# Kernel optimization log

Measured on AMD Instinct MI355X. Metric: run time of the kernel, lower is better.

The kernel has to match this reference:

```python
import jax, jax.numpy as jnp
import numpy as np

EMBED = 512  # scale uses embed_size**-0.5 per the original forward (NOT head_size)


def setup_inputs() -> dict:
    key = jax.random.key(0)
    k1, k2, k3, k4 = jax.random.split(key, 4)
    B, T, D, H = 8, 4096, EMBED, 64
    inputs = jax.random.normal(k1, (B, T, D), dtype=jnp.float32)
    Wq = jax.random.normal(k2, (D, H), dtype=jnp.float32) * (D ** -0.5)
    Wk = jax.random.normal(k3, (D, H), dtype=jnp.float32) * (D ** -0.5)
    Wv = jax.random.normal(k4, (D, H), dtype=jnp.float32) * (D ** -0.5)
    return {"inputs": inputs, "Wq": Wq, "Wk": Wk, "Wv": Wv}


def reference(inputs, Wq, Wk, Wv):
    # inputs: [B, T, D]; Wq/Wk/Wv: [D, H]
    B, T, D = inputs.shape
    q = inputs @ Wq  # [B, T, H]
    k = inputs @ Wk  # [B, T, H]
    v = inputs @ Wv  # [B, T, H]
    scale = jnp.asarray(D, inputs.dtype) ** -0.5  # original scales by embed_size**-0.5
    scores = jnp.einsum('bth,bsh->bts', q, k) * scale  # [B, T, T]
    causal = jnp.arange(T)[:, None] >= jnp.arange(T)[None, :]  # lower-triangular
    scores = jnp.where(causal, scores, jnp.asarray(-jnp.inf, scores.dtype))
    weights = jax.nn.softmax(scores, axis=-1)
    # dropout is identity in eval mode
    return weights @ v  # [B, T, H]
```

## Files before the change

kernel.cpp:

```cpp
#include <hip/hip_runtime.h>
#include <hip/hip_bf16.h>
#include <math.h>

#define TSEQ 4096
#define NB 8
#define DEM 512
#define HD 64
#define KP 66
#define VP 34
#define WIP 136
#define WIMG 26624
#define QSZ ((size_t)NB * TSEQ * HD)
#define SLOTS_PER_B 144

typedef __attribute__((ext_vector_type(8))) short short8;
typedef __attribute__((ext_vector_type(4))) short short4v;
typedef __attribute__((ext_vector_type(4))) float float4v;
typedef __attribute__((ext_vector_type(16))) float f32x16;

__device__ __forceinline__ short f2bf(float f) {
    union { float f; unsigned u; } v; v.f = f;
    unsigned r = v.u + 0x7fffu + ((v.u >> 16) & 1u);
    return (short)(r >> 16);
}

__device__ __forceinline__ short8 pack8(float4 a, float4 b) {
    union { short8 s; __hip_bfloat162 h[4]; } u;
    u.h[0] = __float22bfloat162_rn(make_float2(a.x, a.y));
    u.h[1] = __float22bfloat162_rn(make_float2(a.z, a.w));
    u.h[2] = __float22bfloat162_rn(make_float2(b.x, b.y));
    u.h[3] = __float22bfloat162_rn(make_float2(b.z, b.w));
    return u.s;
}

__device__ __forceinline__ int pkbf2(float x, float y) {
    union { __hip_bfloat162 h; int i; } u;
    u.h = __float22bfloat162_rn(make_float2(x, y));
    return u.i;
}

__device__ __forceinline__ short8 mk8(int a, int b, int c, int d) {
    union { short8 s; int i[4]; } u;
    u.i[0] = a; u.i[1] = b; u.i[2] = c; u.i[3] = d;
    return u.s;
}

__device__ __forceinline__ void gload_lds16(const void* g, void* l) {
    __builtin_amdgcn_global_load_lds(
        (const __attribute__((address_space(1))) unsigned int*)g,
        (__attribute__((address_space(3))) unsigned int*)l,
        16, 0, 0);
}

__device__ __host__ __forceinline__ int slot_base(int mq) {
    int a = mq >> 2, r = mq & 3;
    return (a + 1) * (2 * a + r);
}

__global__ __launch_bounds__(256) void wtr_kernel(
    const float* __restrict__ Wq, const float* __restrict__ Wk,
    const float* __restrict__ Wv, short* __restrict__ wimg)
{
    __shared__ float t[64][65];
    const int tid = threadIdx.x;
    const int kb = blockIdx.x;
    const int k0 = kb * 64;
    const int m = blockIdx.y;
    const int c = kb >> 1, half = kb & 1;
    const float* W = (m == 0) ? Wq : ((m == 1) ? Wk : Wv);
    const float sc = (m == 0) ? (0.044194173824159216f * 1.4426950408889634f)
                              : 1.0f;

#pragma unroll
    for (int i = 0; i < 4; ++i) {
        int f = tid + 256 * i;
        int k = f >> 4, n4 = (f & 15) * 4;
        float4 wv = *(const float4*)&W[(k0 + k) * HD + n4];
        t[k][n4 + 0] = wv.x; t[k][n4 + 1] = wv.y;
        t[k][n4 + 2] = wv.z; t[k][n4 + 3] = wv.w;
    }
    __syncthreads();
#pragma unroll
    for (int i = 0; i < 4; ++i) {
        int f = tid + 256 * i;
        int n = f >> 4, k4 = (f & 15) * 4;
        short4v o;
        o[0] = f2bf(t[k4 + 0][n] * sc);
        o[1] = f2bf(t[k4 + 1][n] * sc);
        o[2] = f2bf(t[k4 + 2][n] * sc);
        o[3] = f2bf(t[k4 + 3][n] * sc);
        *(short4v*)&wimg[c * WIMG + (64 * m + n) * WIP + half * 64 + k4] = o;
    }
}

__global__ __launch_bounds__(256, 3) void qkv_mfma(
    const float* __restrict__ x, const short* __restrict__ wimg,
    short* __restrict__ q, short* __restrict__ k, short* __restrict__ vt)
{
    __shared__ alignas(16) short wlds[WIMG];

    const int tid = threadIdx.x;
    const int w = tid >> 6;
    const int l15 = tid & 15;
    const int quad = (tid >> 4) & 3;
    const int rbase = blockIdx.x * 64 + w * 16 + l15;

    const float* xr = x + (size_t)rbase * DEM;
    float4v acc[12] = {};

    float4 xa[4], xb[4];
#pragma unroll
    for (int ks = 0; ks < 4; ++ks) {
        xa[ks] = *(const float4*)&xr[ks * 32 + quad * 8];
        xb[ks] = *(const float4*)&xr[ks * 32 + quad * 8 + 4];
    }

    for (int c = 0; c < 4; ++c) {
        __syncthreads();
        {
            const char* gsrc = (const char*)(wimg + c * WIMG) + tid * 16;
            char* ldst = (char*)wlds + tid * 16;
#pragma unroll
            for (int i = 0; i < 13; ++i)
                gload_lds16(gsrc + i * 4096, ldst + i * 4096);
        }
        short8 xv[4];
#pragma unroll
        for (int ks = 0; ks < 4; ++ks) xv[ks] = pack8(xa[ks], xb[ks]);
        __syncthreads();

        if (c + 1 < 4) {
#pragma unroll
            for (int ks = 0; ks < 4; ++ks) {
                xa[ks] = *(const float4*)&xr[(c + 1) * 128 + ks * 32 + quad * 8];
                xb[ks] = *(const float4*)&xr[(c + 1) * 128 + ks * 32 + quad * 8 + 4];
            }
        }

#pragma unroll
        for (int ks = 0; ks < 4; ++ks) {
            const int lk = ks * 32 + quad * 8;
#pragma unroll
            for (int mt = 0; mt < 12; ++mt) {
                short8 wf = *(const short8*)&wlds[(mt * 16 + l15) * WIP + lk];
                acc[mt] = __builtin_amdgcn_mfma_f32_16x16x32_bf16(wf, xv[ks], acc[mt], 0, 0, 0);
            }
        }
    }

#pragma unroll
    for (int mt = 0; mt < 8; ++mt) {
        short* dst = (mt < 4) ? q : k;
        short4v o;
        o[0] = f2bf(acc[mt][0]); o[1] = f2bf(acc[mt][1]);
        o[2] = f2bf(acc[mt][2]); o[3] = f2bf(acc[mt][3]);
        *(short4v*)&dst[(size_t)rbase * HD + (mt & 3) * 16 + quad * 4] = o;
    }
    const int b = rbase >> 12, t = rbase & (TSEQ - 1);
#pragma unroll
    for (int mt = 8; mt < 12; ++mt) {
#pragma unroll
        for (int reg = 0; reg < 4; ++reg) {
            int d = (mt - 8) * 16 + quad * 4 + reg;
            vt[((size_t)(b * HD + d)) * TSEQ + t] = f2bf(acc[mt][reg]);
        }
    }
}

__global__ __launch_bounds__(64, 3) void flash_mfma(
    const short* __restrict__ qw, const short* __restrict__ kw,
    const short* __restrict__ vtw, float* __restrict__ out,
    float* __restrict__ pO, float* __restrict__ stS)
{
    __shared__ short kt[32 * KP];
    __shared__ short vl[64 * VP];

    const int lane = threadIdx.x;
    const int q5 = lane & 31;
    const int hi = lane >> 5;
    const int bx = blockIdx.x;
    const int b = bx & 7;
    const int r = bx >> 3;
    const int w = r & 3;
    const int idx = r >> 2;

    int mq, j;
    if (idx < 120) {
        int t = idx;
        mq = 31; j = 0;
#pragma unroll 1
        for (int mm = 31; mm >= 3; --mm) {
            int f = (mm + 1) >> 2;
            if (t < f) { mq = mm; j = t; break; }
            t -= f;
        }
    } else {
        int t = idx - 120;
        int kc = t >> 3, p = t & 7;
        mq = (30 - kc) - 4 * p;
        j = (mq + 1) >> 2;
    }
    const int r0 = mq * 128;
    const int ss0 = 16 * j;
    const int ssend = min(16 * (j + 1), 4 * mq + w + 1);
    const int slot = b * SLOTS_PER_B + slot_base(mq) + j;
    const int qrow = r0 + w * 32 + q5;

    short8 qf[4];
    {
        const short* qp = qw + ((size_t)(b * TSEQ + qrow)) * HD + hi * 8;
#pragma unroll
        for (int ks = 0; ks < 4; ++ks) qf[ks] = *(const short8*)(qp + ks * 16);
    }

    f32x16 O0 = {}, O1 = {};
    float l_lane = 0.f;

    const short* kbase = kw + (size_t)b * TSEQ * HD;
    const short* vbase = vtw + (size_t)b * HD * TSEQ;
    const int krow = lane >> 3, kc8 = (lane & 7) * 8;
    const int vrow = lane >> 2, vc8 = (lane & 3) * 8;

    short8 pk0, pk1, pk2, pk3, pv0, pv1, pv2, pv3;
    {
        const short* kg = kbase + (size_t)(ss0 * 32) * HD;
        const short* vg = vbase + ss0 * 32;
        pk0 = *(const short8*)(kg + (krow +  0) * HD + kc8);
        pk1 = *(const short8*)(kg + (krow +  8) * HD + kc8);
        pk2 = *(const short8*)(kg + (krow + 16) * HD + kc8);
        pk3 = *(const short8*)(kg + (krow + 24) * HD + kc8);
        pv0 = *(const short8*)(vg + (size_t)(vrow +  0) * TSEQ + vc8);
        pv1 = *(const short8*)(vg + (size_t)(vrow + 16) * TSEQ + vc8);
        pv2 = *(const short8*)(vg + (size_t)(vrow + 32) * TSEQ + vc8);
        pv3 = *(const short8*)(vg + (size_t)(vrow + 48) * TSEQ + vc8);
    }

    for (int ss = ss0; ss < ssend; ++ss) {
        __syncthreads();
        *(short8*)&kt[(krow +  0) * KP + kc8] = pk0;
        *(short8*)&kt[(krow +  8) * KP + kc8] = pk1;
        *(short8*)&kt[(krow + 16) * KP + kc8] = pk2;
        *(short8*)&kt[(krow + 24) * KP + kc8] = pk3;
        *(short8*)&vl[(vrow +  0) * VP + vc8] = pv0;
        *(short8*)&vl[(vrow + 16) * VP + vc8] = pv1;
        *(short8*)&vl[(vrow + 32) * VP + vc8] = pv2;
        *(short8*)&vl[(vrow + 48) * VP + vc8] = pv3;
        __syncthreads();

        if (ss + 1 < ssend) {
            const short* kg = kbase + (size_t)((ss + 1) * 32) * HD;
            const short* vg = vbase + (ss + 1) * 32;
            pk0 = *(const short8*)(kg + (krow +  0) * HD + kc8);
            pk1 = *(const short8*)(kg + (krow +  8) * HD + kc8);
            pk2 = *(const short8*)(kg + (krow + 16) * HD + kc8);
            pk3 = *(const short8*)(kg + (krow + 24) * HD + kc8);
            pv0 = *(const short8*)(vg + (size_t)(vrow +  0) * TSEQ + vc8);
            pv1 = *(const short8*)(vg + (size_t)(vrow + 16) * TSEQ + vc8);
            pv2 = *(const short8*)(vg + (size_t)(vrow + 32) * TSEQ + vc8);
            pv3 = *(const short8*)(vg + (size_t)(vrow + 48) * TSEQ + vc8);
        }

        f32x16 S = {};
#pragma unroll
        for (int ks = 0; ks < 4; ++ks) {
            short8 a = *(const short8*)&kt[q5 * KP + ks * 16 + hi * 8];
            S = __builtin_amdgcn_mfma_f32_32x32x16_bf16(a, qf[ks], S, 0, 0, 0);
        }

        if (ss * 32 + 31 > r0 + w * 32) {
#pragma unroll
            for (int reg = 0; reg < 16; ++reg) {
                int key = ss * 32 + (reg & 3) + 8 * (reg >> 2) + 4 * hi;
                if (key > qrow) S[reg] = -INFINITY;
            }
        }

        float p[16];
#pragma unroll
        for (int reg = 0; reg < 16; ++reg) {
            p[reg] = __builtin_amdgcn_exp2f(S[reg]);
            l_lane += p[reg];
        }
        int dd[4][2];
#pragma unroll
        for (int a = 0; a < 4; ++a) {
            dd[a][0] = pkbf2(p[4 * a + 0], p[4 * a + 1]);
            dd[a][1] = pkbf2(p[4 * a + 2], p[4 * a + 3]);
        }
        int ra0 = __shfl_xor(hi ? dd[0][0] : dd[1][0], 32, 64);
        int ra1 = __shfl_xor(hi ? dd[0][1] : dd[1][1], 32, 64);
        int rb0 = __shfl_xor(hi ? dd[2][0] : dd[3][0], 32, 64);
        int rb1 = __shfl_xor(hi ? dd[2][1] : dd[3][1], 32, 64);
        short8 PA0 = hi ? mk8(ra0, ra1, dd[1][0], dd[1][1])
                        : mk8(dd[0][0], dd[0][1], ra0, ra1);
        short8 PA1 = hi ? mk8(rb0, rb1, dd[3][0], dd[3][1])
                        : mk8(dd[2][0], dd[2][1], rb0, rb1);

#pragma unroll
        for (int kr = 0; kr < 2; ++kr) {
            short8 pa = kr ? PA1 : PA0;
            short8 v0 = *(const short8*)&vl[(q5)      * VP + kr * 16 + hi * 8];
            short8 v1 = *(const short8*)&vl[(32 + q5) * VP + kr * 16 + hi * 8];
            O0 = __builtin_amdgcn_mfma_f32_32x32x16_bf16(pa, v0, O0, 0, 0, 0);
            O1 = __builtin_amdgcn_mfma_f32_32x32x16_bf16(pa, v1, O1, 0, 0, 0);
        }
    }

    const float ltot = l_lane + __shfl_xor(l_lane, 32, 64);

    if (mq <= 3) {
        float inv = 1.0f / ltot;
#pragma unroll
        for (int reg = 0; reg < 16; ++reg) {
            int qloc = (reg & 3) + 8 * (reg >> 2) + 4 * hi;
            float ir = __shfl(inv, qloc, 64);
            size_t rowb = (size_t)(b * TSEQ + r0 + w * 32 + qloc) * HD + q5;
            out[rowb]      = O0[reg] * ir;
            out[rowb + 32] = O1[reg] * ir;
        }
    } else {
        float* dest = pO + ((size_t)slot * 128 + w * 32) * HD + q5;
#pragma unroll
        for (int reg = 0; reg < 16; ++reg) {
            int qloc = (reg & 3) + 8 * (reg >> 2) + 4 * hi;
            dest[(size_t)qloc * HD]      = O0[reg];
            dest[(size_t)qloc * HD + 32] = O1[reg];
        }
        if (hi == 0) stS[slot * 128 + w * 32 + q5] = ltot;
    }
}

__global__ __launch_bounds__(256) void merge_kernel(
    float* __restrict__ out, const float* __restrict__ pO,
    const float* __restrict__ stS)
{
    const int tid = threadIdx.x;
    const int bx = blockIdx.x;
    const int b = bx / 56, loc = bx - b * 56;
    const int t = 512 + loc * 64 + (tid >> 2);
    const int dq = (tid & 3) * 16;
    const int mq = t >> 7, rr = t & 127;
    const int nseg = (mq + 4) >> 2;
    const int sb = b * SLOTS_PER_B + slot_base(mq);

    float denom = 0.f;
    for (int s = 0; s < nseg; ++s) denom += stS[(sb + s) * 128 + rr];
    float inv = 1.0f / denom;

    float4 o[4] = {};
    for (int s = 0; s < nseg; ++s) {
        const float4* pp = (const float4*)
            &pO[((size_t)(sb + s) * 128 + rr) * HD + dq];
#pragma unroll
        for (int i = 0; i < 4; ++i) {
            float4 p = pp[i];
            o[i].x += p.x; o[i].y += p.y;
            o[i].z += p.z; o[i].w += p.w;
        }
    }
    float4* op = (float4*)&out[((size_t)b * TSEQ + t) * HD + dq];
#pragma unroll
    for (int i = 0; i < 4; ++i) {
        o[i].x *= inv; o[i].y *= inv; o[i].z *= inv; o[i].w *= inv;
        op[i] = o[i];
    }
}

extern "C" void kernel_launch(void* const* d_in, const int* in_sizes, int n_in,
                              void* d_out, int out_size, void* d_ws, size_t ws_size,
                              hipStream_t stream) {
    const float* x  = (const float*)d_in[0];
    const float* Wq = (const float*)d_in[1];
    const float* Wk = (const float*)d_in[2];
    const float* Wv = (const float*)d_in[3];
    float* out = (float*)d_out;

    short* q  = (short*)d_ws;
    short* k  = q + QSZ;
    short* vt = k + QSZ;
    short* wimg = vt + QSZ;
    float* pO = (float*)(wimg + 4 * WIMG);
    float* stS = pO + (size_t)NB * SLOTS_PER_B * 128 * HD;

    wtr_kernel<<<dim3(8, 3), 256, 0, stream>>>(Wq, Wk, Wv, wimg);
    qkv_mfma<<<dim3(NB * TSEQ / 64), 256, 0, stream>>>(x, wimg, q, k, vt);
    flash_mfma<<<dim3(NB * SLOTS_PER_B * 4), 64, 0, stream>>>(q, k, vt, out, pO, stS);
    merge_kernel<<<dim3(448), 256, 0, stream>>>(out, pO, stS);
}
```

Before: 154.4 us.

## Process two 32-row query groups per flash wavefront to reuse K/V tiles

Each single-wave flash block now handles 64 query rows (two 32-row groups) instead of 32. Each staged K and V tile in LDS is reused for two QK and PV MFMA passes, and the grid is halved. This removes half of the global K/V loads and LDS staging per query, at the cost of doubled accumulator registers (the occupancy hint is dropped), fewer blocks, and some extra masked work on diagonal tiles.

```diff
diff --git a/kernel.cpp b/kernel.cpp
--- a/kernel.cpp
+++ b/kernel.cpp
@@ -167,7 +167,7 @@
     }
 }
 
-__global__ __launch_bounds__(64, 3) void flash_mfma(
+__global__ __launch_bounds__(64) void flash_mfma(
     const short* __restrict__ qw, const short* __restrict__ kw,
     const short* __restrict__ vtw, float* __restrict__ out,
     float* __restrict__ pO, float* __restrict__ stS)
@@ -181,8 +181,8 @@
     const int bx = blockIdx.x;
     const int b = bx & 7;
     const int r = bx >> 3;
-    const int w = r & 3;
-    const int idx = r >> 2;
+    const int w = r & 1;
+    const int idx = r >> 1;
 
     int mq, j;
     if (idx < 120) {
@@ -202,19 +202,19 @@
     }
     const int r0 = mq * 128;
     const int ss0 = 16 * j;
-    const int ssend = min(16 * (j + 1), 4 * mq + w + 1);
+    const int ssend = min(16 * (j + 1), 4 * mq + 2 * w + 2);
     const int slot = b * SLOTS_PER_B + slot_base(mq) + j;
-    const int qrow = r0 + w * 32 + q5;
-
-    short8 qf[4];
-    {
-        const short* qp = qw + ((size_t)(b * TSEQ + qrow)) * HD + hi * 8;
-#pragma unroll
-        for (int ks = 0; ks < 4; ++ks) qf[ks] = *(const short8*)(qp + ks * 16);
-    }
-
-    f32x16 O0 = {}, O1 = {};
-    float l_lane = 0.f;
+
+    short8 qf[2][4];
+#pragma unroll
+    for (int g = 0; g < 2; ++g) {
+        const short* qp = qw + ((size_t)(b * TSEQ + r0 + 64 * w + 32 * g + q5)) * HD + hi * 8;
+#pragma unroll
+        for (int ks = 0; ks < 4; ++ks) qf[g][ks] = *(const short8*)(qp + ks * 16);
+    }
+
+    f32x16 O[2][2] = {};
+    float l_lane[2] = {0.f, 0.f};
 
     const short* kbase = kw + (size_t)b * TSEQ * HD;
     const short* vbase = vtw + (size_t)b * HD * TSEQ;
@@ -260,73 +260,88 @@
             pv3 = *(const short8*)(vg + (size_t)(vrow + 48) * TSEQ + vc8);
         }
 
-        f32x16 S = {};
-#pragma unroll
-        for (int ks = 0; ks < 4; ++ks) {
-            short8 a = *(const short8*)&kt[q5 * KP + ks * 16 + hi * 8];
-            S = __builtin_amdgcn_mfma_f32_32x32x16_bf16(a, qf[ks], S, 0, 0, 0);
-        }
-
-        if (ss * 32 + 31 > r0 + w * 32) {
+#pragma unroll
+        for (int g = 0; g < 2; ++g) {
+            const int grow = r0 + 64 * w + 32 * g;
+            const int qg = grow + q5;
+
+            f32x16 S = {};
+#pragma unroll
+            for (int ks = 0; ks < 4; ++ks) {
+                short8 a = *(const short8*)&kt[q5 * KP + ks * 16 + hi * 8];
+                S = __builtin_amdgcn_mfma_f32_32x32x16_bf16(a, qf[g][ks], S, 0, 0, 0);
+            }
+
+            if (ss * 32 + 31 > grow) {
+#pragma unroll
+                for (int reg = 0; reg < 16; ++reg) {
+                    int key = ss * 32 + (reg & 3) + 8 * (reg >> 2) + 4 * hi;
+                    if (key > qg) S[reg] = -INFINITY;
+                }
+            }
+
+            float p[16];
 #pragma unroll
             for (int reg = 0; reg < 16; ++reg) {
-                int key = ss * 32 + (reg & 3) + 8 * (reg >> 2) + 4 * hi;
-                if (key > qrow) S[reg] = -INFINITY;
-            }
-        }
-
-        float p[16];
-#pragma unroll
-        for (int reg = 0; reg < 16; ++reg) {
-            p[reg] = __builtin_amdgcn_exp2f(S[reg]);
-            l_lane += p[reg];
-        }
-        int dd[4][2];
-#pragma unroll
-        for (int a = 0; a < 4; ++a) {
-            dd[a][0] = pkbf2(p[4 * a + 0], p[4 * a + 1]);
-            dd[a][1] = pkbf2(p[4 * a + 2], p[4 * a + 3]);
-        }
-        int ra0 = __shfl_xor(hi ? dd[0][0] : dd[1][0], 32, 64);
-        int ra1 = __shfl_xor(hi ? dd[0][1] : dd[1][1], 32, 64);
-        int rb0 = __shfl_xor(hi ? dd[2][0] : dd[3][0], 32, 64);
-        int rb1 = __shfl_xor(hi ? dd[2][1] : dd[3][1], 32, 64);
-        short8 PA0 = hi ? mk8(ra0, ra1, dd[1][0], dd[1][1])
-                        : mk8(dd[0][0], dd[0][1], ra0, ra1);
-        short8 PA1 = hi ? mk8(rb0, rb1, dd[3][0], dd[3][1])
-                        : mk8(dd[2][0], dd[2][1], rb0, rb1);
-
-#pragma unroll
-        for (int kr = 0; kr < 2; ++kr) {
-            short8 pa = kr ? PA1 : PA0;
-            short8 v0 = *(const short8*)&vl[(q5)      * VP + kr * 16 + hi * 8];
-            short8 v1 = *(const short8*)&vl[(32 + q5) * VP + kr * 16 + hi * 8];
-            O0 = __builtin_amdgcn_mfma_f32_32x32x16_bf16(pa, v0, O0, 0, 0, 0);
-            O1 = __builtin_amdgcn_mfma_f32_32x32x16_bf16(pa, v1, O1, 0, 0, 0);
-        }
-    }
-
-    const float ltot = l_lane + __shfl_xor(l_lane, 32, 64);
+                p[reg] = __builtin_amdgcn_exp2f(S[reg]);
+                l_lane[g] += p[reg];
+            }
+            int dd[4][2];
+#pragma unroll
+            for (int a = 0; a < 4; ++a) {
+                dd[a][0] = pkbf2(p[4 * a + 0], p[4 * a + 1]);
+                dd[a][1] = pkbf2(p[4 * a + 2], p[4 * a + 3]);
+            }
+            int ra0 = __shfl_xor(hi ? dd[0][0] : dd[1][0], 32, 64);
+            int ra1 = __shfl_xor(hi ? dd[0][1] : dd[1][1], 32, 64);
+            int rb0 = __shfl_xor(hi ? dd[2][0] : dd[3][0], 32, 64);
+            int rb1 = __shfl_xor(hi ? dd[2][1] : dd[3][1], 32, 64);
+            short8 PA0 = hi ? mk8(ra0, ra1, dd[1][0], dd[1][1])
+                            : mk8(dd[0][0], dd[0][1], ra0, ra1);
+            short8 PA1 = hi ? mk8(rb0, rb1, dd[3][0], dd[3][1])
+                            : mk8(dd[2][0], dd[2][1], rb0, rb1);
+
+#pragma unroll
+            for (int kr = 0; kr < 2; ++kr) {
+                short8 pa = kr ? PA1 : PA0;
+                short8 v0 = *(const short8*)&vl[(q5)      * VP + kr * 16 + hi * 8];
+                short8 v1 = *(const short8*)&vl[(32 + q5) * VP + kr * 16 + hi * 8];
+                O[g][0] = __builtin_amdgcn_mfma_f32_32x32x16_bf16(pa, v0, O[g][0], 0, 0, 0);
+                O[g][1] = __builtin_amdgcn_mfma_f32_32x32x16_bf16(pa, v1, O[g][1], 0, 0, 0);
+            }
+        }
+    }
+
+    float ltot[2];
+#pragma unroll
+    for (int g = 0; g < 2; ++g)
+        ltot[g] = l_lane[g] + __shfl_xor(l_lane[g], 32, 64);
 
     if (mq <= 3) {
-        float inv = 1.0f / ltot;
-#pragma unroll
-        for (int reg = 0; reg < 16; ++reg) {
-            int qloc = (reg & 3) + 8 * (reg >> 2) + 4 * hi;
-            float ir = __shfl(inv, qloc, 64);
-            size_t rowb = (size_t)(b * TSEQ + r0 + w * 32 + qloc) * HD + q5;
-            out[rowb]      = O0[reg] * ir;
-            out[rowb + 32] = O1[reg] * ir;
+#pragma unroll
+        for (int g = 0; g < 2; ++g) {
+            float inv = 1.0f / ltot[g];
+#pragma unroll
+            for (int reg = 0; reg < 16; ++reg) {
+                int qloc = (reg & 3) + 8 * (reg >> 2) + 4 * hi;
+                float ir = __shfl(inv, qloc, 64);
+                size_t rowb = (size_t)(b * TSEQ + r0 + 64 * w + 32 * g + qloc) * HD + q5;
+                out[rowb]      = O[g][0][reg] * ir;
+                out[rowb + 32] = O[g][1][reg] * ir;
+            }
         }
     } else {
-        float* dest = pO + ((size_t)slot * 128 + w * 32) * HD + q5;
-#pragma unroll
-        for (int reg = 0; reg < 16; ++reg) {
-            int qloc = (reg & 3) + 8 * (reg >> 2) + 4 * hi;
-            dest[(size_t)qloc * HD]      = O0[reg];
-            dest[(size_t)qloc * HD + 32] = O1[reg];
-        }
-        if (hi == 0) stS[slot * 128 + w * 32 + q5] = ltot;
+#pragma unroll
+        for (int g = 0; g < 2; ++g) {
+            float* dest = pO + ((size_t)slot * 128 + w * 64 + 32 * g) * HD + q5;
+#pragma unroll
+            for (int reg = 0; reg < 16; ++reg) {
+                int qloc = (reg & 3) + 8 * (reg >> 2) + 4 * hi;
+                dest[(size_t)qloc * HD]      = O[g][0][reg];
+                dest[(size_t)qloc * HD + 32] = O[g][1][reg];
+            }
+            if (hi == 0) stS[slot * 128 + w * 64 + 32 * g + q5] = ltot[g];
+        }
     }
 }
 
@@ -384,6 +399,6 @@
 
     wtr_kernel<<<dim3(8, 3), 256, 0, stream>>>(Wq, Wk, Wv, wimg);
     qkv_mfma<<<dim3(NB * TSEQ / 64), 256, 0, stream>>>(x, wimg, q, k, vt);
-    flash_mfma<<<dim3(NB * SLOTS_PER_B * 4), 64, 0, stream>>>(q, k, vt, out, pO, stS);
+    flash_mfma<<<dim3(NB * SLOTS_PER_B * 2), 64, 0, stream>>>(q, k, vt, out, pO, stS);
     merge_kernel<<<dim3(448), 256, 0, stream>>>(out, pO, stS);
 }
```

New measurement: 157.8 us. 1.02x slower.

## Load K/V fragments directly from global into registers, drop LDS staging

Applied to the files above, without the earlier changes.

The flash attention loop no longer stages K and V tiles through shared memory with two barriers per step. Each lane instead loads its MFMA operand fragments straight from global memory into registers, using a two-buffer ping-pong to prefetch the next tile while the current one is computed. The launch-bounds occupancy hint is also relaxed. This removes the LDS traffic and __syncthreads overhead. In exchange it adds more register pressure and gives up the wide coalesced global loads the cooperative staging provided; for V the per-lane 16-byte loads are strided by TSEQ.

```diff
diff --git a/kernel.cpp b/kernel.cpp
--- a/kernel.cpp
+++ b/kernel.cpp
@@ -6,8 +6,6 @@
 #define NB 8
 #define DEM 512
 #define HD 64
-#define KP 66
-#define VP 34
 #define WIP 136
 #define WIMG 26624
 #define QSZ ((size_t)NB * TSEQ * HD)
@@ -167,14 +165,11 @@
     }
 }
 
-__global__ __launch_bounds__(64, 3) void flash_mfma(
+__global__ __launch_bounds__(64) void flash_mfma(
     const short* __restrict__ qw, const short* __restrict__ kw,
     const short* __restrict__ vtw, float* __restrict__ out,
     float* __restrict__ pO, float* __restrict__ stS)
 {
-    __shared__ short kt[32 * KP];
-    __shared__ short vl[64 * VP];
-
     const int lane = threadIdx.x;
     const int q5 = lane & 31;
     const int hi = lane >> 5;
@@ -216,56 +211,31 @@
     f32x16 O0 = {}, O1 = {};
     float l_lane = 0.f;
 
-    const short* kbase = kw + (size_t)b * TSEQ * HD;
-    const short* vbase = vtw + (size_t)b * HD * TSEQ;
-    const int krow = lane >> 3, kc8 = (lane & 7) * 8;
-    const int vrow = lane >> 2, vc8 = (lane & 3) * 8;
-
-    short8 pk0, pk1, pk2, pk3, pv0, pv1, pv2, pv3;
-    {
-        const short* kg = kbase + (size_t)(ss0 * 32) * HD;
-        const short* vg = vbase + ss0 * 32;
-        pk0 = *(const short8*)(kg + (krow +  0) * HD + kc8);
-        pk1 = *(const short8*)(kg + (krow +  8) * HD + kc8);
-        pk2 = *(const short8*)(kg + (krow + 16) * HD + kc8);
-        pk3 = *(const short8*)(kg + (krow + 24) * HD + kc8);
-        pv0 = *(const short8*)(vg + (size_t)(vrow +  0) * TSEQ + vc8);
-        pv1 = *(const short8*)(vg + (size_t)(vrow + 16) * TSEQ + vc8);
-        pv2 = *(const short8*)(vg + (size_t)(vrow + 32) * TSEQ + vc8);
-        pv3 = *(const short8*)(vg + (size_t)(vrow + 48) * TSEQ + vc8);
-    }
-
-    for (int ss = ss0; ss < ssend; ++ss) {
-        __syncthreads();
-        *(short8*)&kt[(krow +  0) * KP + kc8] = pk0;
-        *(short8*)&kt[(krow +  8) * KP + kc8] = pk1;
-        *(short8*)&kt[(krow + 16) * KP + kc8] = pk2;
-        *(short8*)&kt[(krow + 24) * KP + kc8] = pk3;
-        *(short8*)&vl[(vrow +  0) * VP + vc8] = pv0;
-        *(short8*)&vl[(vrow + 16) * VP + vc8] = pv1;
-        *(short8*)&vl[(vrow + 32) * VP + vc8] = pv2;
-        *(short8*)&vl[(vrow + 48) * VP + vc8] = pv3;
-        __syncthreads();
-
-        if (ss + 1 < ssend) {
-            const short* kg = kbase + (size_t)((ss + 1) * 32) * HD;
-            const short* vg = vbase + (ss + 1) * 32;
-            pk0 = *(const short8*)(kg + (krow +  0) * HD + kc8);
-            pk1 = *(const short8*)(kg + (krow +  8) * HD + kc8);
-            pk2 = *(const short8*)(kg + (krow + 16) * HD + kc8);
-            pk3 = *(const short8*)(kg + (krow + 24) * HD + kc8);
-            pv0 = *(const short8*)(vg + (size_t)(vrow +  0) * TSEQ + vc8);
-            pv1 = *(const short8*)(vg + (size_t)(vrow + 16) * TSEQ + vc8);
-            pv2 = *(const short8*)(vg + (size_t)(vrow + 32) * TSEQ + vc8);
-            pv3 = *(const short8*)(vg + (size_t)(vrow + 48) * TSEQ + vc8);
-        }
-
+    const short* kfb  = kw  + ((size_t)(b * TSEQ) + q5) * HD + hi * 8;
+    const short* vfb0 = vtw + ((size_t)(b * HD + q5)) * TSEQ + hi * 8;
+    const short* vfb1 = vtw + ((size_t)(b * HD + 32 + q5)) * TSEQ + hi * 8;
+
+    short8 ka[4], va[4], kb_[4], vb_[4];
+
+    auto LOADF = [&](short8* kf, short8* vf, int ss) {
+        const short* kp  = kfb  + (size_t)ss * 32 * HD;
+        const short* vp0 = vfb0 + ss * 32;
+        const short* vp1 = vfb1 + ss * 32;
+        kf[0] = *(const short8*)(kp);
+        kf[1] = *(const short8*)(kp + 16);
+        kf[2] = *(const short8*)(kp + 32);
+        kf[3] = *(const short8*)(kp + 48);
+        vf[0] = *(const short8*)(vp0);
+        vf[1] = *(const short8*)(vp0 + 16);
+        vf[2] = *(const short8*)(vp1);
+        vf[3] = *(const short8*)(vp1 + 16);
+    };
+
+    auto STEP = [&](const short8* kf, const short8* vf, int ss) {
         f32x16 S = {};
 #pragma unroll
-        for (int ks = 0; ks < 4; ++ks) {
-            short8 a = *(const short8*)&kt[q5 * KP + ks * 16 + hi * 8];
-            S = __builtin_amdgcn_mfma_f32_32x32x16_bf16(a, qf[ks], S, 0, 0, 0);
-        }
+        for (int ks = 0; ks < 4; ++ks)
+            S = __builtin_amdgcn_mfma_f32_32x32x16_bf16(kf[ks], qf[ks], S, 0, 0, 0);
 
         if (ss * 32 + 31 > r0 + w * 32) {
 #pragma unroll
@@ -296,15 +266,22 @@
         short8 PA1 = hi ? mk8(rb0, rb1, dd[3][0], dd[3][1])
                         : mk8(dd[2][0], dd[2][1], rb0, rb1);
 
-#pragma unroll
-        for (int kr = 0; kr < 2; ++kr) {
-            short8 pa = kr ? PA1 : PA0;
-            short8 v0 = *(const short8*)&vl[(q5)      * VP + kr * 16 + hi * 8];
-            short8 v1 = *(const short8*)&vl[(32 + q5) * VP + kr * 16 + hi * 8];
-            O0 = __builtin_amdgcn_mfma_f32_32x32x16_bf16(pa, v0, O0, 0, 0, 0);
-            O1 = __builtin_amdgcn_mfma_f32_32x32x16_bf16(pa, v1, O1, 0, 0, 0);
-        }
-    }
+        O0 = __builtin_amdgcn_mfma_f32_32x32x16_bf16(PA0, vf[0], O0, 0, 0, 0);
+        O0 = __builtin_amdgcn_mfma_f32_32x32x16_bf16(PA1, vf[1], O0, 0, 0, 0);
+        O1 = __builtin_amdgcn_mfma_f32_32x32x16_bf16(PA0, vf[2], O1, 0, 0, 0);
+        O1 = __builtin_amdgcn_mfma_f32_32x32x16_bf16(PA1, vf[3], O1, 0, 0, 0);
+    };
+
+    LOADF(ka, va, ss0);
+    int ss = ss0;
+#pragma unroll 1
+    for (; ss + 1 < ssend; ss += 2) {
+        LOADF(kb_, vb_, ss + 1);
+        STEP(ka, va, ss);
+        if (ss + 2 < ssend) LOADF(ka, va, ss + 2);
+        STEP(kb_, vb_, ss + 1);
+    }
+    if (ss < ssend) STEP(ka, va, ss);
 
     const float ltot = l_lane + __shfl_xor(l_lane, 32, 64);
 
```

Result: slower. 183.9 us (+19.1%).
